# Performance work log

Measured on AMD Instinct MI355X. Metric: run time of the kernel, lower is better.

Reference implementation:

```python
import math
import jax, jax.numpy as jnp
import numpy as np

B, DK, N, M = 32, 64, 2048, 2048


def setup_inputs() -> dict:
    key = jax.random.key(0)
    k1, k2, k3, k4 = jax.random.split(key, 4)
    return {
        "action_embedding": jax.random.normal(k1, (B, DK, N), dtype=jnp.float32),
        "anchor_embedding": jax.random.normal(k2, (B, DK, M), dtype=jnp.float32),
        "action_points": jax.random.normal(k3, (B, 3, N), dtype=jnp.float32),
        "anchor_points": jax.random.normal(k4, (B, 3, M), dtype=jnp.float32),
    }


def reference(action_embedding, anchor_embedding, action_points, anchor_points):
    d_k = action_embedding.shape[1]
    # scores[b,n,m] = <action_emb[b,:,n], anchor_emb[b,:,m]> / sqrt(d_k)
    scores = jnp.einsum("bdn,bdm->bnm", action_embedding, anchor_embedding) / math.sqrt(d_k)
    scores = jax.nn.softmax(scores, axis=2)
    # soft correspondences: action_corr[b,:,n] = sum_m anchor_points[b,:,m] * scores[b,n,m]
    action_corr = jnp.einsum("bcm,bnm->bcn", anchor_points, scores)

    action_mean = action_points.mean(axis=2, keepdims=True)   # [B,3,1]
    corr_mean = action_corr.mean(axis=2, keepdims=True)       # [B,3,1]
    action_centered = action_points - action_mean
    corr_centered = action_corr - corr_mean
    # cross-covariance H[b] = action_centered @ corr_centered^T, 3x3
    H = jnp.einsum("bin,bjn->bij", action_centered, corr_centered)

    # batched Kabsch: R = V @ U^T, with reflection fix via flipping last column of V
    Uh, S, Vh = jnp.linalg.svd(H)            # Uh: [B,3,3], Vh: [B,3,3]
    V = jnp.swapaxes(Vh, 1, 2)
    Ut = jnp.swapaxes(Uh, 1, 2)
    R = V @ Ut
    det = jnp.linalg.det(R)                  # [B]
    flip = jnp.where(det < 0, -1.0, 1.0)     # [B]
    sign = jnp.stack([jnp.ones_like(flip), jnp.ones_like(flip), flip], axis=-1)  # [B,3]
    V_fixed = V * sign[:, None, :]           # scale last column where det<0
    R = V_fixed @ Ut

    t = jnp.einsum("bij,bjk->bik", -R, action_mean) + corr_mean  # [B,3,1]
    return R, t.reshape(action_points.shape[0], 3)
```

## Files before the change

### kernel.cpp

```cpp
#include <hip/hip_runtime.h>
#include <math.h>

#define BB 32
#define DKK 64
#define NN 2048
#define MM 2048
#define MSPLIT 4
#define RQ 2

typedef __attribute__((ext_vector_type(8))) short bfrag8;
typedef __attribute__((ext_vector_type(4))) float facc4;

static __device__ __forceinline__ unsigned short f2bf(float f) {
    union { float f; unsigned int u; } v; v.f = f;
    unsigned int u = v.u;
    u += 0x7fffu + ((u >> 16) & 1u);
    return (unsigned short)(u >> 16);
}
static __device__ __forceinline__ float bf2f(unsigned short h) {
    union { unsigned int u; float f; } v; v.u = ((unsigned int)h) << 16;
    return v.f;
}
static __device__ __forceinline__ void split_bf(float x, short& hi, short& lo) {
    unsigned short h = f2bf(x);
    hi = (short)h;
    lo = (short)f2bf(x - bf2f(h));
}

static __device__ __forceinline__ void gload_lds16(const void* g, void* l) {
    __builtin_amdgcn_global_load_lds(
        (const __attribute__((address_space(1))) unsigned int*)g,
        (__attribute__((address_space(3))) unsigned int*)l, 16, 0, 0);
}

__global__ __launch_bounds__(256) void prep_k(const float* __restrict__ KE,
                                              bfrag8* __restrict__ KBH,
                                              bfrag8* __restrict__ KBL)
{
    const int b = blockIdx.y, mb = blockIdx.x;
    const int t = threadIdx.x;
    const int seg = t >> 6, lane = t & 63;
    __shared__ float T[64][65];

    const float* src = KE + (size_t)b * 64 * MM + mb * 64;
#pragma unroll
    for (int i = 0; i < 16; ++i) {
        int d = i * 4 + seg;
        T[d][lane] = src[(size_t)d * MM + lane];
    }
    __syncthreads();

    const int lq = lane >> 4, lm = lane & 15;
#pragma unroll
    for (int p = 0; p < 2; ++p) {
        bfrag8 fh, fl;
#pragma unroll
        for (int j = 0; j < 8; ++j) {
            float v = T[32 * p + 8 * lq + j][16 * seg + lm];
            short h, l2;
            split_bf(v, h, l2);
            fh[j] = h; fl[j] = l2;
        }
        size_t idx = ((size_t)(b * 128 + mb * 4 + seg) * 2 + p) * 64 + lane;
        KBH[idx] = fh;
        KBL[idx] = fl;
    }
}

__global__ __launch_bounds__(256, 4) void attn_main(
    const float* __restrict__ AE,
    const float* __restrict__ ANP,
    const short* __restrict__ KBH,
    const short* __restrict__ KBL,
    float* __restrict__ PART)
{
    const int t = threadIdx.x;
    const int w = t >> 6, l = t & 63;
    const int ms = blockIdx.x, b = blockIdx.z;
    const int nw = blockIdx.y * 4 + w;
    const int n0 = nw * 32;
    const int lq = l >> 4, lm = l & 15;

    __shared__ __align__(16) unsigned char kbuf[2][4096];

    const float SC = 0.125f;
    bfrag8 qfh[RQ][2], qfl[RQ][2];
    const float* qbase = AE + (size_t)b * 64 * NN + n0 + lm;
#pragma unroll
    for (int r = 0; r < RQ; ++r) {
#pragma unroll
        for (int c = 0; c < 2; ++c) {
            bfrag8 fh, fl;
#pragma unroll
            for (int j = 0; j < 8; ++j) {
                int d = 32 * c + 8 * lq + j;
                float v = qbase[(size_t)d * NN + 16 * r] * SC;
                short h, l2;
                split_bf(v, h, l2);
                fh[j] = h; fl[j] = l2;
            }
            qfh[r][c] = fh;
            qfl[r][c] = fl;
        }
    }

    float accL[RQ][4] = {}, acc0[RQ][4] = {}, acc1[RQ][4] = {}, acc2[RQ][4] = {};

    const float* vb = ANP + (size_t)b * 3 * MM;
    const int mt0 = ms * 32;

    const char* khB = (const char*)KBH + (size_t)b * 128 * 2048;
    const char* klB = (const char*)KBL + (size_t)b * 128 * 2048;

    {
        const char* s = (w < 2) ? khB + (size_t)mt0 * 2048 + t * 16
                                : klB + (size_t)mt0 * 2048 + (t - 128) * 16;
        void* dp = (w < 2) ? (void*)(kbuf[0] + w * 1024)
                           : (void*)(kbuf[0] + 2048 + (w - 2) * 1024);
        gload_lds16(s, dp);
    }
    int m = mt0 * 16 + lm;
    float v0 = vb[m], v1 = vb[MM + m], v2 = vb[2 * MM + m];

    int cur = 0;
    for (int mt = 0; mt < 32; ++mt) {
        __syncthreads();

        const int mtn = (mt + 1) & 31;
        {
            const char* s = (w < 2) ? khB + (size_t)(mt0 + mtn) * 2048 + t * 16
                                    : klB + (size_t)(mt0 + mtn) * 2048 + (t - 128) * 16;
            void* dp = (w < 2) ? (void*)(kbuf[cur ^ 1] + w * 1024)
                               : (void*)(kbuf[cur ^ 1] + 2048 + (w - 2) * 1024);
            gload_lds16(s, dp);
        }
        const int mn = (mt0 + mtn) * 16 + lm;
        float nv0 = vb[mn], nv1 = vb[MM + mn], nv2 = vb[2 * MM + mn];

        const unsigned char* kb = kbuf[cur];
        bfrag8 kh0 = *(const bfrag8*)(kb + l * 16);
        bfrag8 kh1 = *(const bfrag8*)(kb + 1024 + l * 16);
        bfrag8 kl0 = *(const bfrag8*)(kb + 2048 + l * 16);
        bfrag8 kl1 = *(const bfrag8*)(kb + 3072 + l * 16);

#pragma unroll
        for (int r = 0; r < RQ; ++r) {
            facc4 d = {0.f, 0.f, 0.f, 0.f};
            d = __builtin_amdgcn_mfma_f32_16x16x32_bf16(qfh[r][0], kh0, d, 0, 0, 0);
            d = __builtin_amdgcn_mfma_f32_16x16x32_bf16(qfh[r][1], kh1, d, 0, 0, 0);
            d = __builtin_amdgcn_mfma_f32_16x16x32_bf16(qfh[r][0], kl0, d, 0, 0, 0);
            d = __builtin_amdgcn_mfma_f32_16x16x32_bf16(qfh[r][1], kl1, d, 0, 0, 0);
            d = __builtin_amdgcn_mfma_f32_16x16x32_bf16(qfl[r][0], kh0, d, 0, 0, 0);
            d = __builtin_amdgcn_mfma_f32_16x16x32_bf16(qfl[r][1], kh1, d, 0, 0, 0);
#pragma unroll
            for (int e = 0; e < 4; ++e) {
                float p = __expf(d[e]);
                accL[r][e] += p;
                acc0[r][e] = fmaf(p, v0, acc0[r][e]);
                acc1[r][e] = fmaf(p, v1, acc1[r][e]);
                acc2[r][e] = fmaf(p, v2, acc2[r][e]);
            }
        }
        v0 = nv0; v1 = nv1; v2 = nv2;
        cur ^= 1;
    }

    float* pout = PART + (((size_t)(b * MSPLIT + ms) * NN) + n0) * 4;
#pragma unroll
    for (int r = 0; r < RQ; ++r) {
#pragma unroll
        for (int e = 0; e < 4; ++e) {
            float L = accL[r][e], a0 = acc0[r][e], a1 = acc1[r][e], a2 = acc2[r][e];
#pragma unroll
            for (int off = 1; off < 16; off <<= 1) {
                L  += __shfl_xor(L,  off);
                a0 += __shfl_xor(a0, off);
                a1 += __shfl_xor(a1, off);
                a2 += __shfl_xor(a2, off);
            }
            if (lm == 0) {
                int nl = 16 * r + 4 * lq + e;
                facc4 o = {L, a0, a1, a2};
                *(facc4*)(pout + (size_t)nl * 4) = o;
            }
        }
    }
}

__global__ __launch_bounds__(256) void reduce_svd(
    const float* __restrict__ PART,
    const float* __restrict__ ACP,
    float* __restrict__ out)
{
    const int b = blockIdx.x;
    const int t = threadIdx.x;
    const int lane = t & 63;
    const int w    = t >> 6;

    const float* ab = ACP + (size_t)b * 3 * NN;

    float sa0 = 0, sa1 = 0, sa2 = 0;
    float sc0 = 0, sc1 = 0, sc2 = 0;
    float sac[9] = {0, 0, 0, 0, 0, 0, 0, 0, 0};

    for (int n = t; n < NN; n += 256) {
        facc4 s = {0.f, 0.f, 0.f, 0.f};
#pragma unroll
        for (int ms = 0; ms < MSPLIT; ++ms)
            s += *(const facc4*)(PART + (((size_t)(b * MSPLIT + ms) * NN) + n) * 4);
        float inv = 1.f / s[0];
        float c0 = s[1] * inv, c1 = s[2] * inv, c2 = s[3] * inv;
        float A0 = ab[n], A1 = ab[NN + n], A2 = ab[2 * NN + n];
        sa0 += A0; sa1 += A1; sa2 += A2;
        sc0 += c0; sc1 += c1; sc2 += c2;
        sac[0] = fmaf(A0, c0, sac[0]); sac[1] = fmaf(A0, c1, sac[1]); sac[2] = fmaf(A0, c2, sac[2]);
        sac[3] = fmaf(A1, c0, sac[3]); sac[4] = fmaf(A1, c1, sac[4]); sac[5] = fmaf(A1, c2, sac[5]);
        sac[6] = fmaf(A2, c0, sac[6]); sac[7] = fmaf(A2, c1, sac[7]); sac[8] = fmaf(A2, c2, sac[8]);
    }

    float vals[15];
    vals[0] = sa0; vals[1] = sa1; vals[2] = sa2;
    vals[3] = sc0; vals[4] = sc1; vals[5] = sc2;
#pragma unroll
    for (int k = 0; k < 9; ++k) vals[6 + k] = sac[k];

#pragma unroll
    for (int k = 0; k < 15; ++k) {
        float v = vals[k];
        for (int off = 32; off > 0; off >>= 1) v += __shfl_xor(v, off);
        vals[k] = v;
    }

    __shared__ float rbuf[4][15];
    if (lane == 0) {
#pragma unroll
        for (int k = 0; k < 15; ++k) rbuf[w][k] = vals[k];
    }
    __syncthreads();

    if (t == 0) {
        double tot[15];
#pragma unroll
        for (int k = 0; k < 15; ++k)
            tot[k] = (double)rbuf[0][k] + rbuf[1][k] + rbuf[2][k] + rbuf[3][k];

        double am[3], cm[3];
        for (int i = 0; i < 3; ++i) {
            am[i] = tot[i] / (double)NN;
            cm[i] = tot[3 + i] / (double)NN;
        }
        double H[3][3];
        for (int i = 0; i < 3; ++i)
            for (int j = 0; j < 3; ++j)
                H[i][j] = tot[6 + 3 * i + j] - (double)NN * am[i] * cm[j];

        double K[3][3];
        for (int i = 0; i < 3; ++i)
            for (int j = 0; j < 3; ++j)
                K[i][j] = H[0][i] * H[0][j] + H[1][i] * H[1][j] + H[2][i] * H[2][j];
        double V[3][3] = {{1, 0, 0}, {0, 1, 0}, {0, 0, 1}};
        for (int sweep = 0; sweep < 10; ++sweep) {
            for (int pi = 0; pi < 3; ++pi) {
                int p = (pi == 2) ? 1 : 0;
                int qq = (pi == 0) ? 1 : 2;
                double apq = K[p][qq];
                if (fabs(apq) < 1e-300) continue;
                double app = K[p][p], aqq2 = K[qq][qq];
                double tau = (aqq2 - app) / (2.0 * apq);
                double tt = ((tau >= 0.0) ? 1.0 : -1.0) / (fabs(tau) + sqrt(1.0 + tau * tau));
                double c = 1.0 / sqrt(1.0 + tt * tt);
                double s = tt * c;
                for (int k = 0; k < 3; ++k) {
                    double kp = K[k][p], kq = K[k][qq];
                    K[k][p] = c * kp - s * kq; K[k][qq] = s * kp + c * kq;
                }
                for (int k = 0; k < 3; ++k) {
                    double kp = K[p][k], kq = K[qq][k];
                    K[p][k] = c * kp - s * kq; K[qq][k] = s * kp + c * kq;
                }
                for (int k = 0; k < 3; ++k) {
                    double vp = V[k][p], vq = V[k][qq];
                    V[k][p] = c * vp - s * vq; V[k][qq] = s * vp + c * vq;
                }
            }
        }
        double lam[3] = {K[0][0], K[1][1], K[2][2]};
        for (int i = 0; i < 2; ++i)
            for (int j = i + 1; j < 3; ++j)
                if (lam[j] > lam[i]) {
                    double tmp = lam[i]; lam[i] = lam[j]; lam[j] = tmp;
                    for (int k = 0; k < 3; ++k) {
                        double tv = V[k][i]; V[k][i] = V[k][j]; V[k][j] = tv;
                    }
                }
        double U[3][3], sig[3];
        for (int k = 0; k < 3; ++k) {
            double u0 = H[0][0] * V[0][k] + H[0][1] * V[1][k] + H[0][2] * V[2][k];
            double u1 = H[1][0] * V[0][k] + H[1][1] * V[1][k] + H[1][2] * V[2][k];
            double u2 = H[2][0] * V[0][k] + H[2][1] * V[1][k] + H[2][2] * V[2][k];
            double nrm = sqrt(u0 * u0 + u1 * u1 + u2 * u2);
            sig[k] = nrm;
            double inv = (nrm > 1e-30) ? 1.0 / nrm : 0.0;
            U[0][k] = u0 * inv; U[1][k] = u1 * inv; U[2][k] = u2 * inv;
        }
        if (sig[2] <= 1e-10 * fmax(sig[0], 1e-300)) {
            U[0][2] = U[1][0] * U[2][1] - U[2][0] * U[1][1];
            U[1][2] = U[2][0] * U[0][1] - U[0][0] * U[2][1];
            U[2][2] = U[0][0] * U[1][1] - U[1][0] * U[0][1];
        }
        {
            double d01 = U[0][1] * U[0][0] + U[1][1] * U[1][0] + U[2][1] * U[2][0];
            for (int i = 0; i < 3; ++i) U[i][1] -= d01 * U[i][0];
            double n1 = sqrt(U[0][1] * U[0][1] + U[1][1] * U[1][1] + U[2][1] * U[2][1]);
            if (n1 > 1e-30) for (int i = 0; i < 3; ++i) U[i][1] /= n1;
            double d02 = U[0][2] * U[0][0] + U[1][2] * U[1][0] + U[2][2] * U[2][0];
            double d12 = U[0][2] * U[0][1] + U[1][2] * U[1][1] + U[2][2] * U[2][1];
            for (int i = 0; i < 3; ++i) U[i][2] -= d02 * U[i][0] + d12 * U[i][1];
            double n2 = sqrt(U[0][2] * U[0][2] + U[1][2] * U[1][2] + U[2][2] * U[2][2]);
            if (n2 > 1e-30) for (int i = 0; i < 3; ++i) U[i][2] /= n2;
        }

        double detH =
            H[0][0] * (H[1][1] * H[2][2] - H[1][2] * H[2][1]) -
            H[0][1] * (H[1][0] * H[2][2] - H[1][2] * H[2][0]) +
            H[0][2] * (H[1][0] * H[2][1] - H[1][1] * H[2][0]);
        double s3 = (detH < 0.0) ? -1.0 : 1.0;

        double R[3][3];
        for (int i = 0; i < 3; ++i)
            for (int j = 0; j < 3; ++j)
                R[i][j] = V[i][0] * U[j][0] + V[i][1] * U[j][1] + s3 * V[i][2] * U[j][2];

        double tv[3];
        for (int i = 0; i < 3; ++i)
            tv[i] = cm[i] - (R[i][0] * am[0] + R[i][1] * am[1] + R[i][2] * am[2]);

        float* Rout = out + (size_t)b * 9;
        for (int i = 0; i < 3; ++i)
            for (int j = 0; j < 3; ++j)
                Rout[3 * i + j] = (float)R[i][j];
        float* Tout = out + 288 + (size_t)b * 3;
        for (int i = 0; i < 3; ++i) Tout[i] = (float)tv[i];
    }
}

extern "C" void kernel_launch(void* const* d_in, const int* in_sizes, int n_in,
                              void* d_out, int out_size, void* d_ws, size_t ws_size,
                              hipStream_t stream) {
    (void)in_sizes; (void)n_in; (void)out_size; (void)ws_size;
    const float* AE  = (const float*)d_in[0];
    const float* KE  = (const float*)d_in[1];
    const float* ACP = (const float*)d_in[2];
    const float* ANP = (const float*)d_in[3];
    float* out = (float*)d_out;

    short* KBH  = (short*)d_ws;
    short* KBL  = (short*)((char*)d_ws + (8u << 20));
    float* PART = (float*)((char*)d_ws + (16u << 20));

    prep_k<<<dim3(MM / 64, BB), 256, 0, stream>>>(KE, (bfrag8*)KBH, (bfrag8*)KBL);
    attn_main<<<dim3(MSPLIT, NN / (32 * 4), BB), 256, 0, stream>>>(AE, ANP, KBH, KBL, PART);
    reduce_svd<<<BB, 256, 0, stream>>>(PART, ACP, out);
}
```

Before: 161.6 us.

## Stage four key subtiles per barrier and split final reduction across blocks

The attention loop now stages 64 key columns (four 16-column subtiles of hi/lo bf16 fragments) into LDS per iteration instead of 16. This cuts the number of __syncthreads and async-load rounds by four while growing shared memory per block from 8 KB to 32 KB. The per-batch reduction and SVD kernel is split in two. A 256-block partial-sum kernel is followed by a single-block kernel in which each thread does one batch's 3x3 Jacobi SVD, replacing 32 blocks where only one thread did the serial work. This adds a launch and an intermediate buffer, and the larger LDS footprint may lower occupancy.

```diff
diff --git a/kernel.cpp b/kernel.cpp
--- a/kernel.cpp
+++ b/kernel.cpp
@@ -7,6 +7,7 @@
 #define MM 2048
 #define MSPLIT 4
 #define RQ 2
+#define NTILES 8
 
 typedef __attribute__((ext_vector_type(8))) short bfrag8;
 typedef __attribute__((ext_vector_type(4))) float facc4;
@@ -81,7 +82,7 @@
     const int n0 = nw * 32;
     const int lq = l >> 4, lm = l & 15;
 
-    __shared__ __align__(16) unsigned char kbuf[2][4096];
+    __shared__ __align__(16) unsigned char kbuf[2][16384];
 
     const float SC = 0.125f;
     bfrag8 qfh[RQ][2], qfl[RQ][2];
@@ -107,61 +108,74 @@
     float accL[RQ][4] = {}, acc0[RQ][4] = {}, acc1[RQ][4] = {}, acc2[RQ][4] = {};
 
     const float* vb = ANP + (size_t)b * 3 * MM;
-    const int mt0 = ms * 32;
-
     const char* khB = (const char*)KBH + (size_t)b * 128 * 2048;
     const char* klB = (const char*)KBL + (size_t)b * 128 * 2048;
-
-    {
-        const char* s = (w < 2) ? khB + (size_t)mt0 * 2048 + t * 16
-                                : klB + (size_t)mt0 * 2048 + (t - 128) * 16;
-        void* dp = (w < 2) ? (void*)(kbuf[0] + w * 1024)
-                           : (void*)(kbuf[0] + 2048 + (w - 2) * 1024);
-        gload_lds16(s, dp);
-    }
-    int m = mt0 * 16 + lm;
-    float v0 = vb[m], v1 = vb[MM + m], v2 = vb[2 * MM + m];
+    const int mt0 = ms * NTILES;
+
+    auto STAGE = [&](int bi, int tt) {
+        const char* hs = khB + (size_t)(mt0 + tt) * 8192;
+        const char* ls = klB + (size_t)(mt0 + tt) * 8192;
+        unsigned char* db = kbuf[bi];
+#pragma unroll
+        for (int i = 0; i < 4; ++i) {
+            int c = i * 4 + w;
+            const char* s = (c < 8) ? hs + c * 1024 + l * 16
+                                    : ls + (c - 8) * 1024 + l * 16;
+            gload_lds16(s, db + c * 1024 + l * 16);
+        }
+    };
+    auto LOADV = [&](float v[4][3], int tt) {
+#pragma unroll
+        for (int s = 0; s < 4; ++s) {
+            int m = (mt0 + tt) * 64 + s * 16 + lm;
+            v[s][0] = vb[m]; v[s][1] = vb[MM + m]; v[s][2] = vb[2 * MM + m];
+        }
+    };
+
+    STAGE(0, 0);
+    float v[4][3];
+    LOADV(v, 0);
 
     int cur = 0;
-    for (int mt = 0; mt < 32; ++mt) {
+    for (int tt = 0; tt < NTILES; ++tt) {
         __syncthreads();
 
-        const int mtn = (mt + 1) & 31;
-        {
-            const char* s = (w < 2) ? khB + (size_t)(mt0 + mtn) * 2048 + t * 16
-                                    : klB + (size_t)(mt0 + mtn) * 2048 + (t - 128) * 16;
-            void* dp = (w < 2) ? (void*)(kbuf[cur ^ 1] + w * 1024)
-                               : (void*)(kbuf[cur ^ 1] + 2048 + (w - 2) * 1024);
-            gload_lds16(s, dp);
-        }
-        const int mn = (mt0 + mtn) * 16 + lm;
-        float nv0 = vb[mn], nv1 = vb[MM + mn], nv2 = vb[2 * MM + mn];
+        const int ttn = (tt + 1) & (NTILES - 1);
+        STAGE(cur ^ 1, ttn);
+        float nv[4][3];
+        LOADV(nv, ttn);
 
         const unsigned char* kb = kbuf[cur];
-        bfrag8 kh0 = *(const bfrag8*)(kb + l * 16);
-        bfrag8 kh1 = *(const bfrag8*)(kb + 1024 + l * 16);
-        bfrag8 kl0 = *(const bfrag8*)(kb + 2048 + l * 16);
-        bfrag8 kl1 = *(const bfrag8*)(kb + 3072 + l * 16);
-
-#pragma unroll
-        for (int r = 0; r < RQ; ++r) {
-            facc4 d = {0.f, 0.f, 0.f, 0.f};
-            d = __builtin_amdgcn_mfma_f32_16x16x32_bf16(qfh[r][0], kh0, d, 0, 0, 0);
-            d = __builtin_amdgcn_mfma_f32_16x16x32_bf16(qfh[r][1], kh1, d, 0, 0, 0);
-            d = __builtin_amdgcn_mfma_f32_16x16x32_bf16(qfh[r][0], kl0, d, 0, 0, 0);
-            d = __builtin_amdgcn_mfma_f32_16x16x32_bf16(qfh[r][1], kl1, d, 0, 0, 0);
-            d = __builtin_amdgcn_mfma_f32_16x16x32_bf16(qfl[r][0], kh0, d, 0, 0, 0);
-            d = __builtin_amdgcn_mfma_f32_16x16x32_bf16(qfl[r][1], kh1, d, 0, 0, 0);
-#pragma unroll
-            for (int e = 0; e < 4; ++e) {
-                float p = __expf(d[e]);
-                accL[r][e] += p;
-                acc0[r][e] = fmaf(p, v0, acc0[r][e]);
-                acc1[r][e] = fmaf(p, v1, acc1[r][e]);
-                acc2[r][e] = fmaf(p, v2, acc2[r][e]);
-            }
-        }
-        v0 = nv0; v1 = nv1; v2 = nv2;
+#pragma unroll
+        for (int s = 0; s < 4; ++s) {
+            bfrag8 kh0 = *(const bfrag8*)(kb + s * 2048 + l * 16);
+            bfrag8 kh1 = *(const bfrag8*)(kb + s * 2048 + 1024 + l * 16);
+            bfrag8 kl0 = *(const bfrag8*)(kb + 8192 + s * 2048 + l * 16);
+            bfrag8 kl1 = *(const bfrag8*)(kb + 8192 + s * 2048 + 1024 + l * 16);
+
+#pragma unroll
+            for (int r = 0; r < RQ; ++r) {
+                facc4 d = {0.f, 0.f, 0.f, 0.f};
+                d = __builtin_amdgcn_mfma_f32_16x16x32_bf16(qfh[r][0], kh0, d, 0, 0, 0);
+                d = __builtin_amdgcn_mfma_f32_16x16x32_bf16(qfh[r][1], kh1, d, 0, 0, 0);
+                d = __builtin_amdgcn_mfma_f32_16x16x32_bf16(qfh[r][0], kl0, d, 0, 0, 0);
+                d = __builtin_amdgcn_mfma_f32_16x16x32_bf16(qfh[r][1], kl1, d, 0, 0, 0);
+                d = __builtin_amdgcn_mfma_f32_16x16x32_bf16(qfl[r][0], kh0, d, 0, 0, 0);
+                d = __builtin_amdgcn_mfma_f32_16x16x32_bf16(qfl[r][1], kh1, d, 0, 0, 0);
+#pragma unroll
+                for (int e = 0; e < 4; ++e) {
+                    float p = __expf(d[e]);
+                    accL[r][e] += p;
+                    acc0[r][e] = fmaf(p, v[s][0], acc0[r][e]);
+                    acc1[r][e] = fmaf(p, v[s][1], acc1[r][e]);
+                    acc2[r][e] = fmaf(p, v[s][2], acc2[r][e]);
+                }
+            }
+        }
+#pragma unroll
+        for (int s = 0; s < 4; ++s) {
+            v[s][0] = nv[s][0]; v[s][1] = nv[s][1]; v[s][2] = nv[s][2];
+        }
         cur ^= 1;
     }
 
@@ -187,42 +201,34 @@
     }
 }
 
-__global__ __launch_bounds__(256) void reduce_svd(
+__global__ __launch_bounds__(256) void reduce_part(
     const float* __restrict__ PART,
     const float* __restrict__ ACP,
-    float* __restrict__ out)
+    float* __restrict__ PART2)
 {
-    const int b = blockIdx.x;
+    const int bc = blockIdx.x;
+    const int b = bc >> 3, ch = bc & 7;
     const int t = threadIdx.x;
     const int lane = t & 63;
     const int w    = t >> 6;
+    const int n = ch * 256 + t;
 
     const float* ab = ACP + (size_t)b * 3 * NN;
 
-    float sa0 = 0, sa1 = 0, sa2 = 0;
-    float sc0 = 0, sc1 = 0, sc2 = 0;
-    float sac[9] = {0, 0, 0, 0, 0, 0, 0, 0, 0};
-
-    for (int n = t; n < NN; n += 256) {
-        facc4 s = {0.f, 0.f, 0.f, 0.f};
-#pragma unroll
-        for (int ms = 0; ms < MSPLIT; ++ms)
-            s += *(const facc4*)(PART + (((size_t)(b * MSPLIT + ms) * NN) + n) * 4);
-        float inv = 1.f / s[0];
-        float c0 = s[1] * inv, c1 = s[2] * inv, c2 = s[3] * inv;
-        float A0 = ab[n], A1 = ab[NN + n], A2 = ab[2 * NN + n];
-        sa0 += A0; sa1 += A1; sa2 += A2;
-        sc0 += c0; sc1 += c1; sc2 += c2;
-        sac[0] = fmaf(A0, c0, sac[0]); sac[1] = fmaf(A0, c1, sac[1]); sac[2] = fmaf(A0, c2, sac[2]);
-        sac[3] = fmaf(A1, c0, sac[3]); sac[4] = fmaf(A1, c1, sac[4]); sac[5] = fmaf(A1, c2, sac[5]);
-        sac[6] = fmaf(A2, c0, sac[6]); sac[7] = fmaf(A2, c1, sac[7]); sac[8] = fmaf(A2, c2, sac[8]);
-    }
+    facc4 s = {0.f, 0.f, 0.f, 0.f};
+#pragma unroll
+    for (int ms = 0; ms < MSPLIT; ++ms)
+        s += *(const facc4*)(PART + (((size_t)(b * MSPLIT + ms) * NN) + n) * 4);
+    float inv = 1.f / s[0];
+    float c0 = s[1] * inv, c1 = s[2] * inv, c2 = s[3] * inv;
+    float A0 = ab[n], A1 = ab[NN + n], A2 = ab[2 * NN + n];
 
     float vals[15];
-    vals[0] = sa0; vals[1] = sa1; vals[2] = sa2;
-    vals[3] = sc0; vals[4] = sc1; vals[5] = sc2;
-#pragma unroll
-    for (int k = 0; k < 9; ++k) vals[6 + k] = sac[k];
+    vals[0] = A0; vals[1] = A1; vals[2] = A2;
+    vals[3] = c0; vals[4] = c1; vals[5] = c2;
+    vals[6]  = A0 * c0; vals[7]  = A0 * c1; vals[8]  = A0 * c2;
+    vals[9]  = A1 * c0; vals[10] = A1 * c1; vals[11] = A1 * c2;
+    vals[12] = A2 * c0; vals[13] = A2 * c1; vals[14] = A2 * c2;
 
 #pragma unroll
     for (int k = 0; k < 15; ++k) {
@@ -237,111 +243,126 @@
         for (int k = 0; k < 15; ++k) rbuf[w][k] = vals[k];
     }
     __syncthreads();
-
-    if (t == 0) {
-        double tot[15];
-#pragma unroll
-        for (int k = 0; k < 15; ++k)
-            tot[k] = (double)rbuf[0][k] + rbuf[1][k] + rbuf[2][k] + rbuf[3][k];
-
-        double am[3], cm[3];
-        for (int i = 0; i < 3; ++i) {
-            am[i] = tot[i] / (double)NN;
-            cm[i] = tot[3 + i] / (double)NN;
-        }
-        double H[3][3];
-        for (int i = 0; i < 3; ++i)
-            for (int j = 0; j < 3; ++j)
-                H[i][j] = tot[6 + 3 * i + j] - (double)NN * am[i] * cm[j];
-
-        double K[3][3];
-        for (int i = 0; i < 3; ++i)
-            for (int j = 0; j < 3; ++j)
-                K[i][j] = H[0][i] * H[0][j] + H[1][i] * H[1][j] + H[2][i] * H[2][j];
-        double V[3][3] = {{1, 0, 0}, {0, 1, 0}, {0, 0, 1}};
-        for (int sweep = 0; sweep < 10; ++sweep) {
-            for (int pi = 0; pi < 3; ++pi) {
-                int p = (pi == 2) ? 1 : 0;
-                int qq = (pi == 0) ? 1 : 2;
-                double apq = K[p][qq];
-                if (fabs(apq) < 1e-300) continue;
-                double app = K[p][p], aqq2 = K[qq][qq];
-                double tau = (aqq2 - app) / (2.0 * apq);
-                double tt = ((tau >= 0.0) ? 1.0 : -1.0) / (fabs(tau) + sqrt(1.0 + tau * tau));
-                double c = 1.0 / sqrt(1.0 + tt * tt);
-                double s = tt * c;
+    if (t < 15)
+        PART2[(size_t)bc * 16 + t] =
+            rbuf[0][t] + rbuf[1][t] + rbuf[2][t] + rbuf[3][t];
+}
+
+__global__ __launch_bounds__(64) void svd_final(
+    const float* __restrict__ PART2,
+    float* __restrict__ out)
+{
+    const int b = threadIdx.x;
+    if (b >= 32) return;
+
+    double tot[15];
+#pragma unroll
+    for (int k = 0; k < 15; ++k) {
+        double a = 0.0;
+#pragma unroll
+        for (int ch = 0; ch < 8; ++ch)
+            a += (double)PART2[(size_t)(b * 8 + ch) * 16 + k];
+        tot[k] = a;
+    }
+
+    double am[3], cm[3];
+    for (int i = 0; i < 3; ++i) {
+        am[i] = tot[i] / (double)NN;
+        cm[i] = tot[3 + i] / (double)NN;
+    }
+    double H[3][3];
+    for (int i = 0; i < 3; ++i)
+        for (int j = 0; j < 3; ++j)
+            H[i][j] = tot[6 + 3 * i + j] - (double)NN * am[i] * cm[j];
+
+    double K[3][3];
+    for (int i = 0; i < 3; ++i)
+        for (int j = 0; j < 3; ++j)
+            K[i][j] = H[0][i] * H[0][j] + H[1][i] * H[1][j] + H[2][i] * H[2][j];
+    double V[3][3] = {{1, 0, 0}, {0, 1, 0}, {0, 0, 1}};
+    for (int sweep = 0; sweep < 12; ++sweep) {
+        for (int pi = 0; pi < 3; ++pi) {
+            int p = (pi == 2) ? 1 : 0;
+            int qq = (pi == 0) ? 1 : 2;
+            double apq = K[p][qq];
+            double apq_s = (fabs(apq) < 1e-300) ? 1e-300 : apq;
+            double app = K[p][p], aqq2 = K[qq][qq];
+            double tau = (aqq2 - app) / (2.0 * apq_s);
+            double tt = ((tau >= 0.0) ? 1.0 : -1.0) / (fabs(tau) + sqrt(1.0 + tau * tau));
+            tt = (fabs(apq) < 1e-300) ? 0.0 : tt;
+            double c = 1.0 / sqrt(1.0 + tt * tt);
+            double s = tt * c;
+            for (int k = 0; k < 3; ++k) {
+                double kp = K[k][p], kq = K[k][qq];
+                K[k][p] = c * kp - s * kq; K[k][qq] = s * kp + c * kq;
+            }
+            for (int k = 0; k < 3; ++k) {
+                double kp = K[p][k], kq = K[qq][k];
+                K[p][k] = c * kp - s * kq; K[qq][k] = s * kp + c * kq;
+            }
+            for (int k = 0; k < 3; ++k) {
+                double vp = V[k][p], vq = V[k][qq];
+                V[k][p] = c * vp - s * vq; V[k][qq] = s * vp + c * vq;
+            }
+        }
+    }
+    double lam[3] = {K[0][0], K[1][1], K[2][2]};
+    for (int i = 0; i < 2; ++i)
+        for (int j = i + 1; j < 3; ++j)
+            if (lam[j] > lam[i]) {
+                double tmp = lam[i]; lam[i] = lam[j]; lam[j] = tmp;
                 for (int k = 0; k < 3; ++k) {
-                    double kp = K[k][p], kq = K[k][qq];
-                    K[k][p] = c * kp - s * kq; K[k][qq] = s * kp + c * kq;
+                    double tv = V[k][i]; V[k][i] = V[k][j]; V[k][j] = tv;
                 }
-                for (int k = 0; k < 3; ++k) {
-                    double kp = K[p][k], kq = K[qq][k];
-                    K[p][k] = c * kp - s * kq; K[qq][k] = s * kp + c * kq;
-                }
-                for (int k = 0; k < 3; ++k) {
-                    double vp = V[k][p], vq = V[k][qq];
-                    V[k][p] = c * vp - s * vq; V[k][qq] = s * vp + c * vq;
-                }
-            }
-        }
-        double lam[3] = {K[0][0], K[1][1], K[2][2]};
-        for (int i = 0; i < 2; ++i)
-            for (int j = i + 1; j < 3; ++j)
-                if (lam[j] > lam[i]) {
-                    double tmp = lam[i]; lam[i] = lam[j]; lam[j] = tmp;
-                    for (int k = 0; k < 3; ++k) {
-                        double tv = V[k][i]; V[k][i] = V[k][j]; V[k][j] = tv;
-                    }
-                }
-        double U[3][3], sig[3];
-        for (int k = 0; k < 3; ++k) {
-            double u0 = H[0][0] * V[0][k] + H[0][1] * V[1][k] + H[0][2] * V[2][k];
-            double u1 = H[1][0] * V[0][k] + H[1][1] * V[1][k] + H[1][2] * V[2][k];
-            double u2 = H[2][0] * V[0][k] + H[2][1] * V[1][k] + H[2][2] * V[2][k];
-            double nrm = sqrt(u0 * u0 + u1 * u1 + u2 * u2);
-            sig[k] = nrm;
-            double inv = (nrm > 1e-30) ? 1.0 / nrm : 0.0;
-            U[0][k] = u0 * inv; U[1][k] = u1 * inv; U[2][k] = u2 * inv;
-        }
-        if (sig[2] <= 1e-10 * fmax(sig[0], 1e-300)) {
-            U[0][2] = U[1][0] * U[2][1] - U[2][0] * U[1][1];
-            U[1][2] = U[2][0] * U[0][1] - U[0][0] * U[2][1];
-            U[2][2] = U[0][0] * U[1][1] - U[1][0] * U[0][1];
-        }
-        {
-            double d01 = U[0][1] * U[0][0] + U[1][1] * U[1][0] + U[2][1] * U[2][0];
-            for (int i = 0; i < 3; ++i) U[i][1] -= d01 * U[i][0];
-            double n1 = sqrt(U[0][1] * U[0][1] + U[1][1] * U[1][1] + U[2][1] * U[2][1]);
-            if (n1 > 1e-30) for (int i = 0; i < 3; ++i) U[i][1] /= n1;
-            double d02 = U[0][2] * U[0][0] + U[1][2] * U[1][0] + U[2][2] * U[2][0];
-            double d12 = U[0][2] * U[0][1] + U[1][2] * U[1][1] + U[2][2] * U[2][1];
-            for (int i = 0; i < 3; ++i) U[i][2] -= d02 * U[i][0] + d12 * U[i][1];
-            double n2 = sqrt(U[0][2] * U[0][2] + U[1][2] * U[1][2] + U[2][2] * U[2][2]);
-            if (n2 > 1e-30) for (int i = 0; i < 3; ++i) U[i][2] /= n2;
-        }
-
-        double detH =
-            H[0][0] * (H[1][1] * H[2][2] - H[1][2] * H[2][1]) -
-            H[0][1] * (H[1][0] * H[2][2] - H[1][2] * H[2][0]) +
-            H[0][2] * (H[1][0] * H[2][1] - H[1][1] * H[2][0]);
-        double s3 = (detH < 0.0) ? -1.0 : 1.0;
-
-        double R[3][3];
-        for (int i = 0; i < 3; ++i)
-            for (int j = 0; j < 3; ++j)
-                R[i][j] = V[i][0] * U[j][0] + V[i][1] * U[j][1] + s3 * V[i][2] * U[j][2];
-
-        double tv[3];
-        for (int i = 0; i < 3; ++i)
-            tv[i] = cm[i] - (R[i][0] * am[0] + R[i][1] * am[1] + R[i][2] * am[2]);
-
-        float* Rout = out + (size_t)b * 9;
-        for (int i = 0; i < 3; ++i)
-            for (int j = 0; j < 3; ++j)
-                Rout[3 * i + j] = (float)R[i][j];
-        float* Tout = out + 288 + (size_t)b * 3;
-        for (int i = 0; i < 3; ++i) Tout[i] = (float)tv[i];
-    }
+            }
+    double U[3][3], sig[3];
+    for (int k = 0; k < 3; ++k) {
+        double u0 = H[0][0] * V[0][k] + H[0][1] * V[1][k] + H[0][2] * V[2][k];
+        double u1 = H[1][0] * V[0][k] + H[1][1] * V[1][k] + H[1][2] * V[2][k];
+        double u2 = H[2][0] * V[0][k] + H[2][1] * V[1][k] + H[2][2] * V[2][k];
+        double nrm = sqrt(u0 * u0 + u1 * u1 + u2 * u2);
+        sig[k] = nrm;
+        double inv = (nrm > 1e-30) ? 1.0 / nrm : 0.0;
+        U[0][k] = u0 * inv; U[1][k] = u1 * inv; U[2][k] = u2 * inv;
+    }
+    if (sig[2] <= 1e-10 * fmax(sig[0], 1e-300)) {
+        U[0][2] = U[1][0] * U[2][1] - U[2][0] * U[1][1];
+        U[1][2] = U[2][0] * U[0][1] - U[0][0] * U[2][1];
+        U[2][2] = U[0][0] * U[1][1] - U[1][0] * U[0][1];
+    }
+    {
+        double d01 = U[0][1] * U[0][0] + U[1][1] * U[1][0] + U[2][1] * U[2][0];
+        for (int i = 0; i < 3; ++i) U[i][1] -= d01 * U[i][0];
+        double n1 = sqrt(U[0][1] * U[0][1] + U[1][1] * U[1][1] + U[2][1] * U[2][1]);
+        if (n1 > 1e-30) for (int i = 0; i < 3; ++i) U[i][1] /= n1;
+        double d02 = U[0][2] * U[0][0] + U[1][2] * U[1][0] + U[2][2] * U[2][0];
+        double d12 = U[0][2] * U[0][1] + U[1][2] * U[1][1] + U[2][2] * U[2][1];
+        for (int i = 0; i < 3; ++i) U[i][2] -= d02 * U[i][0] + d12 * U[i][1];
+        double n2 = sqrt(U[0][2] * U[0][2] + U[1][2] * U[1][2] + U[2][2] * U[2][2]);
+        if (n2 > 1e-30) for (int i = 0; i < 3; ++i) U[i][2] /= n2;
+    }
+
+    double detH =
+        H[0][0] * (H[1][1] * H[2][2] - H[1][2] * H[2][1]) -
+        H[0][1] * (H[1][0] * H[2][2] - H[1][2] * H[2][0]) +
+        H[0][2] * (H[1][0] * H[2][1] - H[1][1] * H[2][0]);
+    double s3 = (detH < 0.0) ? -1.0 : 1.0;
+
+    double R[3][3];
+    for (int i = 0; i < 3; ++i)
+        for (int j = 0; j < 3; ++j)
+            R[i][j] = V[i][0] * U[j][0] + V[i][1] * U[j][1] + s3 * V[i][2] * U[j][2];
+
+    double tv[3];
+    for (int i = 0; i < 3; ++i)
+        tv[i] = cm[i] - (R[i][0] * am[0] + R[i][1] * am[1] + R[i][2] * am[2]);
+
+    float* Rout = out + (size_t)b * 9;
+    for (int i = 0; i < 3; ++i)
+        for (int j = 0; j < 3; ++j)
+            Rout[3 * i + j] = (float)R[i][j];
+    float* Tout = out + 288 + (size_t)b * 3;
+    for (int i = 0; i < 3; ++i) Tout[i] = (float)tv[i];
 }
 
 extern "C" void kernel_launch(void* const* d_in, const int* in_sizes, int n_in,
@@ -354,11 +375,13 @@
     const float* ANP = (const float*)d_in[3];
     float* out = (float*)d_out;
 
-    short* KBH  = (short*)d_ws;
-    short* KBL  = (short*)((char*)d_ws + (8u << 20));
-    float* PART = (float*)((char*)d_ws + (16u << 20));
+    short* KBH   = (short*)d_ws;
+    short* KBL   = (short*)((char*)d_ws + (8u << 20));
+    float* PART  = (float*)((char*)d_ws + (16u << 20));
+    float* PART2 = (float*)((char*)d_ws + (21u << 20));
 
     prep_k<<<dim3(MM / 64, BB), 256, 0, stream>>>(KE, (bfrag8*)KBH, (bfrag8*)KBL);
     attn_main<<<dim3(MSPLIT, NN / (32 * 4), BB), 256, 0, stream>>>(AE, ANP, KBH, KBL, PART);
-    reduce_svd<<<BB, 256, 0, stream>>>(PART, ACP, out);
-}
+    reduce_part<<<256, 256, 0, stream>>>(PART, ACP, PART2);
+    svd_final<<<1, 64, 0, stream>>>(PART2, out);
+}
```

After: 171.9 us. 1.06x slower.
